# Kernel tuning notes

Hardware: AMD Instinct MI355X
Metric: run time of the kernel (lower is better)

The kernel has to match this reference:

```python
import jax, jax.numpy as jnp
import numpy as np
import math

EMBED_DIM = 1024
NUM_HEADS = 16
HEAD_DIM = EMBED_DIM // NUM_HEADS  # 64
MAX_SEQ_LEN = 2048


def rope_tables(max_seq_len, dim):
    pos = jnp.arange(max_seq_len, dtype=jnp.float32)
    div_term = jnp.exp(jnp.arange(0, dim, 2, dtype=jnp.float32) * -(math.log(10000.0) / dim))
    ang = pos[:, None] * div_term[None, :]  # [S, dim//2]
    return jnp.sin(ang), jnp.cos(ang)


def apply_rope(x, sin, cos):
    # x: [B, H, S, D]; sin/cos: [max_seq, D//2]
    S = x.shape[2]
    sin = sin[:S][None, None]  # [1,1,S,D//2]
    cos = cos[:S][None, None]
    x1, x2 = jnp.split(x, 2, axis=-1)
    return jnp.concatenate([cos * x1 - sin * x2, sin * x1 + cos * x2], axis=-1)


def setup_inputs() -> dict:
    key = jax.random.key(0)
    ks = jax.random.split(key, 5)
    B, S, E = 4, 2048, EMBED_DIM
    std = 1.0 / math.sqrt(E)
    x = jax.random.normal(ks[0], (B, S, E), dtype=jnp.float32)
    Wq = jax.random.normal(ks[1], (E, E), dtype=jnp.float32) * std
    Wk = jax.random.normal(ks[2], (E, E), dtype=jnp.float32) * std
    Wv = jax.random.normal(ks[3], (E, E), dtype=jnp.float32) * std
    Wo = jax.random.normal(ks[4], (E, E), dtype=jnp.float32) * std
    return {"x": x, "Wq": Wq, "Wk": Wk, "Wv": Wv, "Wo": Wo}


def reference(x, Wq, Wk, Wv, Wo):
    B, S, E = x.shape
    H, D = NUM_HEADS, HEAD_DIM
    scale = 1.0 / math.sqrt(D)
    sin, cos = rope_tables(MAX_SEQ_LEN, D)

    def split_heads(t):
        return t.reshape(B, S, H, D).transpose(0, 2, 1, 3)  # [B,H,S,D]

    q = split_heads(x @ Wq)
    k = split_heads(x @ Wk)
    v = split_heads(x @ Wv)
    q = apply_rope(q, sin, cos)
    k = apply_rope(k, sin, cos)

    scores = jnp.einsum('bhqd,bhkd->bhqk', q, k) * scale
    causal = jnp.where(jnp.tril(jnp.ones((S, S), dtype=bool)), 0.0, -1e9)
    scores = scores + causal[None, None]
    attn = jax.nn.softmax(scores, axis=-1)
    out = jnp.einsum('bhqk,bhkd->bhqd', attn, v)  # [B,H,S,D]
    out = out.transpose(0, 2, 1, 3).reshape(B, S, E)
    return out @ Wo
```

## Files before the change

### kernel.cpp

```cpp
#include <hip/hip_runtime.h>

#define DEVFN __device__ __forceinline__

typedef __attribute__((ext_vector_type(8))) short bf16x8;
typedef __attribute__((ext_vector_type(4))) float f32x4;
typedef __attribute__((ext_vector_type(16))) float f32x16;

#define MFMA16(a, b, c) __builtin_amdgcn_mfma_f32_16x16x32_bf16(a, b, c, 0, 0, 0)
#define MFMA32(a, b, c) __builtin_amdgcn_mfma_f32_32x32x16_bf16(a, b, c, 0, 0, 0)

DEVFN unsigned short f2bf(float f) {
  union { float f; unsigned u; } v; v.f = f;
  unsigned r = v.u + 0x7FFFu + ((v.u >> 16) & 1u);
  return (unsigned short)(r >> 16);
}
DEVFN unsigned pack2bf(float a, float b) {
  return (unsigned)f2bf(a) | ((unsigned)f2bf(b) << 16);
}
DEVFN unsigned cvtpk(float lo, float hi) {
  unsigned r;
  asm("v_cvt_pk_bf16_f32 %0, %1, %2" : "=v"(r) : "v"(lo), "v"(hi));
  return r;
}
DEVFN void pl32swap(unsigned& a, unsigned& b) {
  asm("v_permlane32_swap_b32 %0, %1" : "+v"(a), "+v"(b));
}
DEVFN void gll16(const void* g, void* l) {
  __builtin_amdgcn_global_load_lds((__attribute__((address_space(1))) void*)g,
                                   (__attribute__((address_space(3))) void*)l,
                                   16, 0, 0);
}


__global__ __launch_bounds__(256) void conv_x_k(const float* __restrict__ x,
                                                unsigned short* __restrict__ xb) {
  int i = (blockIdx.x * 256 + threadIdx.x) * 4;
  float4 v = *(const float4*)(x + i);
  uint2 u;
  u.x = pack2bf(v.x, v.y);
  u.y = pack2bf(v.z, v.w);
  *(uint2*)(xb + i) = u;
}

__global__ __launch_bounds__(256) void transp_k(
    const float* __restrict__ Wq, const float* __restrict__ Wk,
    const float* __restrict__ Wv, const float* __restrict__ Wo,
    unsigned short* __restrict__ Tq, unsigned short* __restrict__ Tk,
    unsigned short* __restrict__ Tv, unsigned short* __restrict__ To) {
  __shared__ unsigned short t[64 * 65];
  int z = blockIdx.z;
  const float* src = (z == 0) ? Wq : (z == 1) ? Wk : (z == 2) ? Wv : Wo;
  unsigned short* dst = (z == 0) ? Tq : (z == 1) ? Tk : (z == 2) ? Tv : To;
  int k0 = blockIdx.x * 64, n0 = blockIdx.y * 64;
  int tid = threadIdx.x;
#pragma unroll
  for (int i = 0; i < 16; ++i) {
    int flat = i * 256 + tid;
    int r = flat >> 6, cc = flat & 63;
    t[cc * 65 + r] = f2bf(src[(size_t)(k0 + r) * 1024 + n0 + cc]);
  }
  __syncthreads();
#pragma unroll
  for (int i = 0; i < 16; ++i) {
    int flat = i * 256 + tid;
    int rr = flat >> 6, cc = flat & 63;
    dst[(size_t)(n0 + rr) * 1024 + k0 + cc] = t[rr * 65 + cc];
  }
}

__global__ __launch_bounds__(256) void rope_k(float2* __restrict__ rtab) {
  int idx = blockIdx.x * 256 + threadIdx.x;
  int s = idx >> 5, j = idx & 31;
  float freq = expf(-0.28782313714981824f * (float)j);
  float ang = (float)s * freq;
  rtab[idx] = make_float2(sinf(ang), cosf(ang));
}

template <int MODE>
__global__ __launch_bounds__(256) void gemm_k(
    const unsigned short* __restrict__ A, const unsigned short* __restrict__ WT,
    void* __restrict__ outp, const float2* __restrict__ rtab) {
  __shared__ unsigned short At[128 * 64];
  __shared__ unsigned short Bt[128 * 64];
  const int tid = threadIdx.x;
  const int w = tid >> 6, lane = tid & 63, g = lane >> 4, c = lane & 15;
  const int wr = w >> 1, wc = w & 1;
  const int m0 = blockIdx.x * 128, n0 = blockIdx.y * 128;

  f32x4 zero = {0.f, 0.f, 0.f, 0.f};
  f32x4 acc[4][4];
#pragma unroll
  for (int i = 0; i < 4; ++i)
#pragma unroll
    for (int j = 0; j < 4; ++j) acc[i][j] = zero;

  for (int k0 = 0; k0 < 1024; k0 += 64) {
#pragma unroll
    for (int p = 0; p < 4; ++p) {
      int i = p * 256 + tid;
      int row = i >> 3, ls = i & 7;
      size_t off = ((size_t)(m0 + row) * 1024 + k0) * 2 + ((ls ^ (row & 7)) << 4);
      gll16((const char*)A + off, (char*)At + p * 4096 + w * 1024);
      size_t offb = ((size_t)(n0 + row) * 1024 + k0) * 2 + ((ls ^ (row & 7)) << 4);
      gll16((const char*)WT + offb, (char*)Bt + p * 4096 + w * 1024);
    }
    __syncthreads();
#pragma unroll
    for (int ks = 0; ks < 2; ++ks) {
      bf16x8 af[4], bfv[4];
#pragma unroll
      for (int am = 0; am < 4; ++am) {
        int row = wr * 64 + am * 16 + c;
        af[am] = *(const bf16x8*)(At + row * 64 + ((((ks << 2) | g) ^ (row & 7)) << 3));
      }
#pragma unroll
      for (int bn = 0; bn < 4; ++bn) {
        int row = wc * 64 + bn * 16 + c;
        bfv[bn] = *(const bf16x8*)(Bt + row * 64 + ((((ks << 2) | g) ^ (row & 7)) << 3));
      }
#pragma unroll
      for (int am = 0; am < 4; ++am)
#pragma unroll
        for (int bn = 0; bn < 4; ++bn)
          acc[am][bn] = MFMA16(af[am], bfv[bn], acc[am][bn]);
    }
    __syncthreads();
  }

  if (MODE == 0) {
    unsigned short* outb = (unsigned short*)outp;
#pragma unroll
    for (int am = 0; am < 4; ++am)
#pragma unroll
      for (int bp = 0; bp < 2; ++bp) {
        int col = n0 + wc * 64 + bp * 16 + c;
        int h = col >> 6, j = col & 63;
#pragma unroll
        for (int r = 0; r < 4; ++r) {
          int row = m0 + wr * 64 + am * 16 + (g << 2) + r;
          int b = row >> 11, s = row & 2047;
          float x1 = acc[am][bp][r], x2 = acc[am][bp + 2][r];
          float2 sc = rtab[s * 32 + j];
          float o1 = (sc.y * x1 - sc.x * x2) * 0.18033688011112042f;
          float o2 = (sc.x * x1 + sc.y * x2) * 0.18033688011112042f;
          size_t base = (((size_t)(b * 16 + h)) * 2048 + s) * 64;
          outb[base + j] = f2bf(o1);
          outb[base + 32 + j] = f2bf(o2);
        }
      }
  } else if (MODE == 1) {
    unsigned short* outb = (unsigned short*)outp;
#pragma unroll
    for (int am = 0; am < 4; ++am)
#pragma unroll
      for (int bp = 0; bp < 2; ++bp) {
        int col = n0 + wc * 64 + bp * 16 + c;
        int h = col >> 6, j = col & 63;
        const int kb = j >> 4, hil = (j >> 3) & 1, el = j & 7;
#pragma unroll
        for (int r = 0; r < 4; ++r) {
          int row = m0 + wr * 64 + am * 16 + (g << 2) + r;
          int b = row >> 11, s = row & 2047;
          float x1 = acc[am][bp][r], x2 = acc[am][bp + 2][r];
          float2 sc = rtab[s * 32 + j];
          float o1 = sc.y * x1 - sc.x * x2;
          float o2 = sc.x * x1 + sc.y * x2;
          size_t base = (size_t)(b * 16 + h) * 131072 + (size_t)(s >> 5) * 2048 +
                        (hil * 32 + (s & 31)) * 8 + el;
          outb[base + kb * 512] = f2bf(o1);
          outb[base + (kb + 2) * 512] = f2bf(o2);
        }
      }
  } else if (MODE == 2) {
    unsigned short* outb = (unsigned short*)outp;
#pragma unroll
    for (int am = 0; am < 4; ++am)
#pragma unroll
      for (int bn = 0; bn < 4; ++bn) {
        int col = n0 + wc * 64 + bn * 16 + c;
        int h = col >> 6, d = col & 63;
        int row0 = m0 + wr * 64 + am * 16 + (g << 2);
        int b = row0 >> 11, s0 = row0 & 2047;
        uint2 u;
        u.x = pack2bf(acc[am][bn][0], acc[am][bn][1]);
        u.y = pack2bf(acc[am][bn][2], acc[am][bn][3]);
        size_t off = (size_t)(b * 16 + h) * 131072 + (size_t)(s0 >> 6) * 4096 +
                     ((s0 >> 4) & 3) * 1024 + (d >> 5) * 512 +
                     (((s0 >> 3) & 1) * 32 + (d & 31)) * 8 + (s0 & 7);
        *(uint2*)(outb + off) = u;
      }
  } else {
    float* outf = (float*)outp;
#pragma unroll
    for (int am = 0; am < 4; ++am)
#pragma unroll
      for (int bn = 0; bn < 4; ++bn)
#pragma unroll
        for (int r = 0; r < 4; ++r)
          outf[(size_t)(m0 + wr * 64 + am * 16 + (g << 2) + r) * 1024 +
               (n0 + wc * 64 + bn * 16 + c)] = acc[am][bn][r];
  }
}

__global__ __launch_bounds__(256, 2) void attn_k(
    const unsigned short* __restrict__ Q, const unsigned short* __restrict__ Kf,
    const unsigned short* __restrict__ Vf, unsigned short* __restrict__ ctx) {
  const int blk = blockIdx.x;
  const int xcd = blk & 7, idx = blk >> 3;
  const int bh = (xcd << 3) + (idx & 7);
  const int pbase = (idx >> 3) << 2;
  const int tid = threadIdx.x;
  const int w = tid >> 6, lane = tid & 63;
  const int hi = lane >> 5, c5 = lane & 31;
  const int P = pbase + w;

  const unsigned short* Qbh = Q + (size_t)bh * 2048 * 64;
  const unsigned short* Kbh = Kf + (size_t)bh * 131072;
  const unsigned short* Vbh = Vf + (size_t)bh * 131072;
  const int b = bh >> 4, h = bh & 15;

  f32x16 zacc;
#pragma unroll
  for (int i = 0; i < 16; ++i) zacc[i] = 0.f;

  auto pass = [&](int U) {
    const int qw = U * 32;
    const int S = (U >> 1) + 1;

    bf16x8 qf[4];
#pragma unroll
    for (int kb = 0; kb < 4; ++kb)
      qf[kb] = *(const bf16x8*)(Qbh + (size_t)(qw + c5) * 64 + kb * 16 + hi * 8);

    f32x16 oacc[2];
    oacc[0] = zacc; oacc[1] = zacc;
    float m_run = -1e30f, l_run = 0.f;

    bf16x8 kfA[2][4], vfA[2][4], kfB[2][4], vfB[2][4];

    auto loadK = [&](int st, bf16x8 (&dst)[2][4]) {
      const unsigned short* kb_ = Kbh + (size_t)st * 4096 + lane * 8;
#pragma unroll
      for (int t = 0; t < 2; ++t)
#pragma unroll
        for (int kb = 0; kb < 4; ++kb)
          dst[t][kb] = *(const bf16x8*)(kb_ + t * 2048 + kb * 512);
    };
    auto loadV = [&](int st, bf16x8 (&dst)[2][4]) {
      const unsigned short* vb_ = Vbh + (size_t)st * 4096 + lane * 8;
#pragma unroll
      for (int kb = 0; kb < 4; ++kb) {
        dst[0][kb] = *(const bf16x8*)(vb_ + kb * 1024);
        dst[1][kb] = *(const bf16x8*)(vb_ + kb * 1024 + 512);
      }
    };

    auto step = [&](int st, bf16x8 (&kfC)[2][4], bf16x8 (&vfC)[2][4],
                    bf16x8 (&kfN)[2][4], bf16x8 (&vfN)[2][4]) {
      f32x16 sacc[2];
      __builtin_amdgcn_s_setprio(1);
#pragma unroll
      for (int t = 0; t < 2; ++t) {
        sacc[t] = MFMA32(kfC[t][0], qf[0], zacc);
#pragma unroll
        for (int kb = 1; kb < 4; ++kb)
          sacc[t] = MFMA32(kfC[t][kb], qf[kb], sacc[t]);
      }
      __builtin_amdgcn_s_setprio(0);

      if (st + 1 < S) {
        loadK(st + 1, kfN);
        loadV(st + 1, vfN);
      }

      if (st == S - 1) {
        const int q = qw + c5;
#pragma unroll
        for (int t = 0; t < 2; ++t) {
          const int kvb = st * 64 + t * 32 + (hi << 2);
#pragma unroll
          for (int i = 0; i < 16; ++i) {
            int kv = kvb + (i & 3) + ((i >> 2) << 3);
            if (kv > q) sacc[t][i] = -1e30f;
          }
        }
      }

      float vmax = fmaxf(sacc[0][0], sacc[0][1]);
#pragma unroll
      for (int t = 0; t < 2; ++t)
#pragma unroll
        for (int i = (t == 0 ? 2 : 0); i < 16; i += 2)
          vmax = fmaxf(vmax, fmaxf(sacc[t][i], sacc[t][i + 1]));
      vmax = fmaxf(vmax, __shfl_xor(vmax, 32, 64));
      if (!__all(vmax <= m_run + 8.0f)) {
        float m_new = fmaxf(m_run, vmax);
        float alpha = exp2f(m_run - m_new);
        l_run *= alpha;
#pragma unroll
        for (int i = 0; i < 16; ++i) {
          oacc[0][i] *= alpha;
          oacc[1][i] *= alpha;
        }
        m_run = m_new;
      }
      float psum = 0.f;
#pragma unroll
      for (int t = 0; t < 2; ++t)
#pragma unroll
        for (int i = 0; i < 16; ++i) {
          float pv = exp2f(sacc[t][i] - m_run);
          sacc[t][i] = pv;
          psum += pv;
        }
      psum += __shfl_xor(psum, 32, 64);
      l_run += psum;

      unsigned pword[4][4];
#pragma unroll
      for (int t = 0; t < 2; ++t) {
        unsigned X[4][2];
#pragma unroll
        for (int u2 = 0; u2 < 4; ++u2)
#pragma unroll
          for (int wp = 0; wp < 2; ++wp)
            X[u2][wp] = cvtpk(sacc[t][u2 * 4 + 2 * wp], sacc[t][u2 * 4 + 2 * wp + 1]);
#pragma unroll
        for (int par = 0; par < 2; ++par) {
          const int kb = 2 * t + par;
#pragma unroll
          for (int wp = 0; wp < 2; ++wp) {
            unsigned a = X[2 * par][wp], b2 = X[2 * par + 1][wp];
            pl32swap(a, b2);
            pword[kb][wp] = a;
            pword[kb][wp + 2] = b2;
          }
        }
      }

      __builtin_amdgcn_s_setprio(1);
#pragma unroll
      for (int kb = 0; kb < 4; ++kb) {
        union { unsigned u[4]; bf16x8 v; } pw;
#pragma unroll
        for (int k2 = 0; k2 < 4; ++k2) pw.u[k2] = pword[kb][k2];
        oacc[0] = MFMA32(vfC[0][kb], pw.v, oacc[0]);
        oacc[1] = MFMA32(vfC[1][kb], pw.v, oacc[1]);
      }
      __builtin_amdgcn_s_setprio(0);
    };

    loadK(0, kfA);
    loadV(0, vfA);
    for (int st = 0; st < S; st += 2) {
      step(st, kfA, vfA, kfB, vfB);
      if (st + 1 < S) step(st + 1, kfB, vfB, kfA, vfA);
    }

    const float linv = 1.f / l_run;
    unsigned short* crow = ctx + ((size_t)(b * 2048 + qw + c5)) * 1024 + h * 64;
#pragma unroll
    for (int dt = 0; dt < 2; ++dt)
#pragma unroll
      for (int u = 0; u < 4; ++u) {
        int d0 = dt * 32 + 8 * u + 4 * hi;
        uint2 o;
        o.x = cvtpk(oacc[dt][4 * u] * linv, oacc[dt][4 * u + 1] * linv);
        o.y = cvtpk(oacc[dt][4 * u + 2] * linv, oacc[dt][4 * u + 3] * linv);
        *(uint2*)(crow + d0) = o;
      }
  };

  pass(P);
  pass(63 - P);
}


extern "C" void kernel_launch(void* const* d_in, const int* in_sizes, int n_in,
                              void* d_out, int out_size, void* d_ws, size_t ws_size,
                              hipStream_t stream) {
  (void)in_sizes; (void)n_in; (void)out_size; (void)ws_size;
  const float* x = (const float*)d_in[0];
  const float* Wq = (const float*)d_in[1];
  const float* Wk = (const float*)d_in[2];
  const float* Wv = (const float*)d_in[3];
  const float* Wo = (const float*)d_in[4];
  char* ws = (char*)d_ws;
  const size_t MiB = 1024 * 1024;
  unsigned short* xb  = (unsigned short*)(ws);
  unsigned short* WTq = (unsigned short*)(ws + 16 * MiB);
  unsigned short* WTk = (unsigned short*)(ws + 18 * MiB);
  unsigned short* WTv = (unsigned short*)(ws + 20 * MiB);
  unsigned short* WTo = (unsigned short*)(ws + 22 * MiB);
  unsigned short* Qb  = (unsigned short*)(ws + 24 * MiB);
  unsigned short* Kfb = (unsigned short*)(ws + 40 * MiB);
  unsigned short* Vfb = (unsigned short*)(ws + 56 * MiB);
  unsigned short* ctx = (unsigned short*)(ws + 72 * MiB);
  float2* rtab = (float2*)(ws + 88 * MiB);

  conv_x_k<<<8192, 256, 0, stream>>>(x, xb);
  transp_k<<<dim3(16, 16, 4), 256, 0, stream>>>(Wq, Wk, Wv, Wo, WTq, WTk, WTv, WTo);
  rope_k<<<256, 256, 0, stream>>>(rtab);
  gemm_k<0><<<dim3(64, 8), 256, 0, stream>>>(xb, WTq, Qb, rtab);
  gemm_k<1><<<dim3(64, 8), 256, 0, stream>>>(xb, WTk, Kfb, rtab);
  gemm_k<2><<<dim3(64, 8), 256, 0, stream>>>(xb, WTv, Vfb, rtab);
  attn_k<<<512, 256, 0, stream>>>(Qb, Kfb, Vfb, ctx);
  gemm_k<3><<<dim3(64, 8), 256, 0, stream>>>(ctx, WTo, d_out, rtab);
}
```

Measured before the change: 184.4 us.

## Fuse QKV GEMM launches and rebalance causal attention work across blocks

The three Q/K/V projection GEMMs become a single launch with a 64x24 grid that picks the weight matrix and epilogue from blockIdx.y. Attention moves from 512 blocks, each running two balanced passes per wave, to 1024 blocks where the four waves of a block share one query-tile pair index and span two heads. Blocks are ordered so the longest causal tiles are issued first. This aims to cut launch gaps and the tail between dependent GEMMs and to raise occupancy and scheduling balance in attention. The cost is that waves within a block now carry unequal work (U=2s versus 2s+1), and the light-first pairing of the old scheme is dropped.

```diff
diff --git a/kernel.cpp b/kernel.cpp
--- a/kernel.cpp
+++ b/kernel.cpp
@@ -76,16 +76,19 @@
   rtab[idx] = make_float2(sinf(ang), cosf(ang));
 }
 
-template <int MODE>
-__global__ __launch_bounds__(256) void gemm_k(
-    const unsigned short* __restrict__ A, const unsigned short* __restrict__ WT,
-    void* __restrict__ outp, const float2* __restrict__ rtab) {
+__global__ __launch_bounds__(256) void gemm_qkv_k(
+    const unsigned short* __restrict__ A, const unsigned short* __restrict__ WTq,
+    const unsigned short* __restrict__ WTk, const unsigned short* __restrict__ WTv,
+    unsigned short* __restrict__ Qb, unsigned short* __restrict__ Kfb,
+    unsigned short* __restrict__ Vfb, const float2* __restrict__ rtab) {
   __shared__ unsigned short At[128 * 64];
   __shared__ unsigned short Bt[128 * 64];
   const int tid = threadIdx.x;
   const int w = tid >> 6, lane = tid & 63, g = lane >> 4, c = lane & 15;
   const int wr = w >> 1, wc = w & 1;
-  const int m0 = blockIdx.x * 128, n0 = blockIdx.y * 128;
+  const int which = blockIdx.y >> 3;
+  const unsigned short* WT = (which == 0) ? WTq : (which == 1) ? WTk : WTv;
+  const int m0 = blockIdx.x * 128, n0 = (blockIdx.y & 7) * 128;
 
   f32x4 zero = {0.f, 0.f, 0.f, 0.f};
   f32x4 acc[4][4];
@@ -127,8 +130,7 @@
     __syncthreads();
   }
 
-  if (MODE == 0) {
-    unsigned short* outb = (unsigned short*)outp;
+  if (which == 0) {
 #pragma unroll
     for (int am = 0; am < 4; ++am)
 #pragma unroll
@@ -144,12 +146,11 @@
           float o1 = (sc.y * x1 - sc.x * x2) * 0.18033688011112042f;
           float o2 = (sc.x * x1 + sc.y * x2) * 0.18033688011112042f;
           size_t base = (((size_t)(b * 16 + h)) * 2048 + s) * 64;
-          outb[base + j] = f2bf(o1);
-          outb[base + 32 + j] = f2bf(o2);
+          Qb[base + j] = f2bf(o1);
+          Qb[base + 32 + j] = f2bf(o2);
         }
       }
-  } else if (MODE == 1) {
-    unsigned short* outb = (unsigned short*)outp;
+  } else if (which == 1) {
 #pragma unroll
     for (int am = 0; am < 4; ++am)
 #pragma unroll
@@ -167,12 +168,11 @@
           float o2 = sc.x * x1 + sc.y * x2;
           size_t base = (size_t)(b * 16 + h) * 131072 + (size_t)(s >> 5) * 2048 +
                         (hil * 32 + (s & 31)) * 8 + el;
-          outb[base + kb * 512] = f2bf(o1);
-          outb[base + (kb + 2) * 512] = f2bf(o2);
+          Kfb[base + kb * 512] = f2bf(o1);
+          Kfb[base + (kb + 2) * 512] = f2bf(o2);
         }
       }
-  } else if (MODE == 2) {
-    unsigned short* outb = (unsigned short*)outp;
+  } else {
 #pragma unroll
     for (int am = 0; am < 4; ++am)
 #pragma unroll
@@ -187,32 +187,85 @@
         size_t off = (size_t)(b * 16 + h) * 131072 + (size_t)(s0 >> 6) * 4096 +
                      ((s0 >> 4) & 3) * 1024 + (d >> 5) * 512 +
                      (((s0 >> 3) & 1) * 32 + (d & 31)) * 8 + (s0 & 7);
-        *(uint2*)(outb + off) = u;
-      }
-  } else {
-    float* outf = (float*)outp;
-#pragma unroll
-    for (int am = 0; am < 4; ++am)
-#pragma unroll
-      for (int bn = 0; bn < 4; ++bn)
-#pragma unroll
-        for (int r = 0; r < 4; ++r)
-          outf[(size_t)(m0 + wr * 64 + am * 16 + (g << 2) + r) * 1024 +
-               (n0 + wc * 64 + bn * 16 + c)] = acc[am][bn][r];
-  }
+        *(uint2*)(Vfb + off) = u;
+      }
+  }
+}
+
+__global__ __launch_bounds__(256) void gemm_o_k(
+    const unsigned short* __restrict__ A, const unsigned short* __restrict__ WT,
+    float* __restrict__ outf) {
+  __shared__ unsigned short At[128 * 64];
+  __shared__ unsigned short Bt[128 * 64];
+  const int tid = threadIdx.x;
+  const int w = tid >> 6, lane = tid & 63, g = lane >> 4, c = lane & 15;
+  const int wr = w >> 1, wc = w & 1;
+  const int m0 = blockIdx.x * 128, n0 = blockIdx.y * 128;
+
+  f32x4 zero = {0.f, 0.f, 0.f, 0.f};
+  f32x4 acc[4][4];
+#pragma unroll
+  for (int i = 0; i < 4; ++i)
+#pragma unroll
+    for (int j = 0; j < 4; ++j) acc[i][j] = zero;
+
+  for (int k0 = 0; k0 < 1024; k0 += 64) {
+#pragma unroll
+    for (int p = 0; p < 4; ++p) {
+      int i = p * 256 + tid;
+      int row = i >> 3, ls = i & 7;
+      size_t off = ((size_t)(m0 + row) * 1024 + k0) * 2 + ((ls ^ (row & 7)) << 4);
+      gll16((const char*)A + off, (char*)At + p * 4096 + w * 1024);
+      size_t offb = ((size_t)(n0 + row) * 1024 + k0) * 2 + ((ls ^ (row & 7)) << 4);
+      gll16((const char*)WT + offb, (char*)Bt + p * 4096 + w * 1024);
+    }
+    __syncthreads();
+#pragma unroll
+    for (int ks = 0; ks < 2; ++ks) {
+      bf16x8 af[4], bfv[4];
+#pragma unroll
+      for (int am = 0; am < 4; ++am) {
+        int row = wr * 64 + am * 16 + c;
+        af[am] = *(const bf16x8*)(At + row * 64 + ((((ks << 2) | g) ^ (row & 7)) << 3));
+      }
+#pragma unroll
+      for (int bn = 0; bn < 4; ++bn) {
+        int row = wc * 64 + bn * 16 + c;
+        bfv[bn] = *(const bf16x8*)(Bt + row * 64 + ((((ks << 2) | g) ^ (row & 7)) << 3));
+      }
+#pragma unroll
+      for (int am = 0; am < 4; ++am)
+#pragma unroll
+        for (int bn = 0; bn < 4; ++bn)
+          acc[am][bn] = MFMA16(af[am], bfv[bn], acc[am][bn]);
+    }
+    __syncthreads();
+  }
+
+#pragma unroll
+  for (int am = 0; am < 4; ++am)
+#pragma unroll
+    for (int bn = 0; bn < 4; ++bn)
+#pragma unroll
+      for (int r = 0; r < 4; ++r)
+        outf[(size_t)(m0 + wr * 64 + am * 16 + (g << 2) + r) * 1024 +
+             (n0 + wc * 64 + bn * 16 + c)] = acc[am][bn][r];
 }
 
 __global__ __launch_bounds__(256, 2) void attn_k(
     const unsigned short* __restrict__ Q, const unsigned short* __restrict__ Kf,
     const unsigned short* __restrict__ Vf, unsigned short* __restrict__ ctx) {
   const int blk = blockIdx.x;
-  const int xcd = blk & 7, idx = blk >> 3;
-  const int bh = (xcd << 3) + (idx & 7);
-  const int pbase = (idx >> 3) << 2;
+  const int xcd = blk & 7, j = blk >> 3;
+  const int hp = j & 3;
+  const int s = 31 - (j >> 2);
   const int tid = threadIdx.x;
   const int w = tid >> 6, lane = tid & 63;
   const int hi = lane >> 5, c5 = lane & 31;
-  const int P = pbase + w;
+  const int bh = xcd * 8 + hp * 2 + (w & 1);
+  const int U = 2 * s + (w >> 1);
+  const int S = s + 1;
+  const int qw = U * 32;
 
   const unsigned short* Qbh = Q + (size_t)bh * 2048 * 64;
   const unsigned short* Kbh = Kf + (size_t)bh * 131072;
@@ -223,156 +276,148 @@
 #pragma unroll
   for (int i = 0; i < 16; ++i) zacc[i] = 0.f;
 
-  auto pass = [&](int U) {
-    const int qw = U * 32;
-    const int S = (U >> 1) + 1;
-
-    bf16x8 qf[4];
-#pragma unroll
-    for (int kb = 0; kb < 4; ++kb)
-      qf[kb] = *(const bf16x8*)(Qbh + (size_t)(qw + c5) * 64 + kb * 16 + hi * 8);
-
-    f32x16 oacc[2];
-    oacc[0] = zacc; oacc[1] = zacc;
-    float m_run = -1e30f, l_run = 0.f;
-
-    bf16x8 kfA[2][4], vfA[2][4], kfB[2][4], vfB[2][4];
-
-    auto loadK = [&](int st, bf16x8 (&dst)[2][4]) {
-      const unsigned short* kb_ = Kbh + (size_t)st * 4096 + lane * 8;
-#pragma unroll
-      for (int t = 0; t < 2; ++t)
-#pragma unroll
-        for (int kb = 0; kb < 4; ++kb)
-          dst[t][kb] = *(const bf16x8*)(kb_ + t * 2048 + kb * 512);
-    };
-    auto loadV = [&](int st, bf16x8 (&dst)[2][4]) {
-      const unsigned short* vb_ = Vbh + (size_t)st * 4096 + lane * 8;
-#pragma unroll
-      for (int kb = 0; kb < 4; ++kb) {
-        dst[0][kb] = *(const bf16x8*)(vb_ + kb * 1024);
-        dst[1][kb] = *(const bf16x8*)(vb_ + kb * 1024 + 512);
-      }
-    };
-
-    auto step = [&](int st, bf16x8 (&kfC)[2][4], bf16x8 (&vfC)[2][4],
-                    bf16x8 (&kfN)[2][4], bf16x8 (&vfN)[2][4]) {
-      f32x16 sacc[2];
-      __builtin_amdgcn_s_setprio(1);
+  bf16x8 qf[4];
+#pragma unroll
+  for (int kb = 0; kb < 4; ++kb)
+    qf[kb] = *(const bf16x8*)(Qbh + (size_t)(qw + c5) * 64 + kb * 16 + hi * 8);
+
+  f32x16 oacc[2];
+  oacc[0] = zacc; oacc[1] = zacc;
+  float m_run = -1e30f, l_run = 0.f;
+
+  bf16x8 kfA[2][4], vfA[2][4], kfB[2][4], vfB[2][4];
+
+  auto loadK = [&](int st, bf16x8 (&dst)[2][4]) {
+    const unsigned short* kb_ = Kbh + (size_t)st * 4096 + lane * 8;
+#pragma unroll
+    for (int t = 0; t < 2; ++t)
+#pragma unroll
+      for (int kb = 0; kb < 4; ++kb)
+        dst[t][kb] = *(const bf16x8*)(kb_ + t * 2048 + kb * 512);
+  };
+  auto loadV = [&](int st, bf16x8 (&dst)[2][4]) {
+    const unsigned short* vb_ = Vbh + (size_t)st * 4096 + lane * 8;
+#pragma unroll
+    for (int kb = 0; kb < 4; ++kb) {
+      dst[0][kb] = *(const bf16x8*)(vb_ + kb * 1024);
+      dst[1][kb] = *(const bf16x8*)(vb_ + kb * 1024 + 512);
+    }
+  };
+
+  auto step = [&](int st, bf16x8 (&kfC)[2][4], bf16x8 (&vfC)[2][4],
+                  bf16x8 (&kfN)[2][4], bf16x8 (&vfN)[2][4]) {
+    f32x16 sacc[2];
+    __builtin_amdgcn_s_setprio(1);
+#pragma unroll
+    for (int t = 0; t < 2; ++t) {
+      sacc[t] = MFMA32(kfC[t][0], qf[0], zacc);
+#pragma unroll
+      for (int kb = 1; kb < 4; ++kb)
+        sacc[t] = MFMA32(kfC[t][kb], qf[kb], sacc[t]);
+    }
+    __builtin_amdgcn_s_setprio(0);
+
+    if (st + 1 < S) {
+      loadK(st + 1, kfN);
+      loadV(st + 1, vfN);
+    }
+
+    if (st == S - 1) {
+      const int q = qw + c5;
 #pragma unroll
       for (int t = 0; t < 2; ++t) {
-        sacc[t] = MFMA32(kfC[t][0], qf[0], zacc);
-#pragma unroll
-        for (int kb = 1; kb < 4; ++kb)
-          sacc[t] = MFMA32(kfC[t][kb], qf[kb], sacc[t]);
-      }
-      __builtin_amdgcn_s_setprio(0);
-
-      if (st + 1 < S) {
-        loadK(st + 1, kfN);
-        loadV(st + 1, vfN);
-      }
-
-      if (st == S - 1) {
-        const int q = qw + c5;
-#pragma unroll
-        for (int t = 0; t < 2; ++t) {
-          const int kvb = st * 64 + t * 32 + (hi << 2);
-#pragma unroll
-          for (int i = 0; i < 16; ++i) {
-            int kv = kvb + (i & 3) + ((i >> 2) << 3);
-            if (kv > q) sacc[t][i] = -1e30f;
-          }
+        const int kvb = st * 64 + t * 32 + (hi << 2);
+#pragma unroll
+        for (int i = 0; i < 16; ++i) {
+          int kv = kvb + (i & 3) + ((i >> 2) << 3);
+          if (kv > q) sacc[t][i] = -1e30f;
         }
       }
-
-      float vmax = fmaxf(sacc[0][0], sacc[0][1]);
-#pragma unroll
-      for (int t = 0; t < 2; ++t)
-#pragma unroll
-        for (int i = (t == 0 ? 2 : 0); i < 16; i += 2)
-          vmax = fmaxf(vmax, fmaxf(sacc[t][i], sacc[t][i + 1]));
-      vmax = fmaxf(vmax, __shfl_xor(vmax, 32, 64));
-      if (!__all(vmax <= m_run + 8.0f)) {
-        float m_new = fmaxf(m_run, vmax);
-        float alpha = exp2f(m_run - m_new);
-        l_run *= alpha;
-#pragma unroll
-        for (int i = 0; i < 16; ++i) {
-          oacc[0][i] *= alpha;
-          oacc[1][i] *= alpha;
+    }
+
+    float vmax = fmaxf(sacc[0][0], sacc[0][1]);
+#pragma unroll
+    for (int t = 0; t < 2; ++t)
+#pragma unroll
+      for (int i = (t == 0 ? 2 : 0); i < 16; i += 2)
+        vmax = fmaxf(vmax, fmaxf(sacc[t][i], sacc[t][i + 1]));
+    vmax = fmaxf(vmax, __shfl_xor(vmax, 32, 64));
+    if (!__all(vmax <= m_run + 8.0f)) {
+      float m_new = fmaxf(m_run, vmax);
+      float alpha = exp2f(m_run - m_new);
+      l_run *= alpha;
+#pragma unroll
+      for (int i = 0; i < 16; ++i) {
+        oacc[0][i] *= alpha;
+        oacc[1][i] *= alpha;
+      }
+      m_run = m_new;
+    }
+    float psum = 0.f;
+#pragma unroll
+    for (int t = 0; t < 2; ++t)
+#pragma unroll
+      for (int i = 0; i < 16; ++i) {
+        float pv = exp2f(sacc[t][i] - m_run);
+        sacc[t][i] = pv;
+        psum += pv;
+      }
+    psum += __shfl_xor(psum, 32, 64);
+    l_run += psum;
+
+    unsigned pword[4][4];
+#pragma unroll
+    for (int t = 0; t < 2; ++t) {
+      unsigned X[4][2];
+#pragma unroll
+      for (int u2 = 0; u2 < 4; ++u2)
+#pragma unroll
+        for (int wp = 0; wp < 2; ++wp)
+          X[u2][wp] = cvtpk(sacc[t][u2 * 4 + 2 * wp], sacc[t][u2 * 4 + 2 * wp + 1]);
+#pragma unroll
+      for (int par = 0; par < 2; ++par) {
+        const int kb = 2 * t + par;
+#pragma unroll
+        for (int wp = 0; wp < 2; ++wp) {
+          unsigned a = X[2 * par][wp], b2 = X[2 * par + 1][wp];
+          pl32swap(a, b2);
+          pword[kb][wp] = a;
+          pword[kb][wp + 2] = b2;
         }
-        m_run = m_new;
-      }
-      float psum = 0.f;
-#pragma unroll
-      for (int t = 0; t < 2; ++t)
-#pragma unroll
-        for (int i = 0; i < 16; ++i) {
-          float pv = exp2f(sacc[t][i] - m_run);
-          sacc[t][i] = pv;
-          psum += pv;
-        }
-      psum += __shfl_xor(psum, 32, 64);
-      l_run += psum;
-
-      unsigned pword[4][4];
-#pragma unroll
-      for (int t = 0; t < 2; ++t) {
-        unsigned X[4][2];
-#pragma unroll
-        for (int u2 = 0; u2 < 4; ++u2)
-#pragma unroll
-          for (int wp = 0; wp < 2; ++wp)
-            X[u2][wp] = cvtpk(sacc[t][u2 * 4 + 2 * wp], sacc[t][u2 * 4 + 2 * wp + 1]);
-#pragma unroll
-        for (int par = 0; par < 2; ++par) {
-          const int kb = 2 * t + par;
-#pragma unroll
-          for (int wp = 0; wp < 2; ++wp) {
-            unsigned a = X[2 * par][wp], b2 = X[2 * par + 1][wp];
-            pl32swap(a, b2);
-            pword[kb][wp] = a;
-            pword[kb][wp + 2] = b2;
-          }
-        }
-      }
-
-      __builtin_amdgcn_s_setprio(1);
-#pragma unroll
-      for (int kb = 0; kb < 4; ++kb) {
-        union { unsigned u[4]; bf16x8 v; } pw;
-#pragma unroll
-        for (int k2 = 0; k2 < 4; ++k2) pw.u[k2] = pword[kb][k2];
-        oacc[0] = MFMA32(vfC[0][kb], pw.v, oacc[0]);
-        oacc[1] = MFMA32(vfC[1][kb], pw.v, oacc[1]);
-      }
-      __builtin_amdgcn_s_setprio(0);
-    };
-
-    loadK(0, kfA);
-    loadV(0, vfA);
-    for (int st = 0; st < S; st += 2) {
-      step(st, kfA, vfA, kfB, vfB);
-      if (st + 1 < S) step(st + 1, kfB, vfB, kfA, vfA);
-    }
-
-    const float linv = 1.f / l_run;
-    unsigned short* crow = ctx + ((size_t)(b * 2048 + qw + c5)) * 1024 + h * 64;
-#pragma unroll
-    for (int dt = 0; dt < 2; ++dt)
-#pragma unroll
-      for (int u = 0; u < 4; ++u) {
-        int d0 = dt * 32 + 8 * u + 4 * hi;
-        uint2 o;
-        o.x = cvtpk(oacc[dt][4 * u] * linv, oacc[dt][4 * u + 1] * linv);
-        o.y = cvtpk(oacc[dt][4 * u + 2] * linv, oacc[dt][4 * u + 3] * linv);
-        *(uint2*)(crow + d0) = o;
-      }
+      }
+    }
+
+    __builtin_amdgcn_s_setprio(1);
+#pragma unroll
+    for (int kb = 0; kb < 4; ++kb) {
+      union { unsigned u[4]; bf16x8 v; } pw;
+#pragma unroll
+      for (int k2 = 0; k2 < 4; ++k2) pw.u[k2] = pword[kb][k2];
+      oacc[0] = MFMA32(vfC[0][kb], pw.v, oacc[0]);
+      oacc[1] = MFMA32(vfC[1][kb], pw.v, oacc[1]);
+    }
+    __builtin_amdgcn_s_setprio(0);
   };
 
-  pass(P);
-  pass(63 - P);
+  loadK(0, kfA);
+  loadV(0, vfA);
+  for (int st = 0; st < S; st += 2) {
+    step(st, kfA, vfA, kfB, vfB);
+    if (st + 1 < S) step(st + 1, kfB, vfB, kfA, vfA);
+  }
+
+  const float linv = 1.f / l_run;
+  unsigned short* crow = ctx + ((size_t)(b * 2048 + qw + c5)) * 1024 + h * 64;
+#pragma unroll
+  for (int dt = 0; dt < 2; ++dt)
+#pragma unroll
+    for (int u = 0; u < 4; ++u) {
+      int d0 = dt * 32 + 8 * u + 4 * hi;
+      uint2 o;
+      o.x = cvtpk(oacc[dt][4 * u] * linv, oacc[dt][4 * u + 1] * linv);
+      o.y = cvtpk(oacc[dt][4 * u + 2] * linv, oacc[dt][4 * u + 3] * linv);
+      *(uint2*)(crow + d0) = o;
+    }
 }
 
 
@@ -401,9 +446,7 @@
   conv_x_k<<<8192, 256, 0, stream>>>(x, xb);
   transp_k<<<dim3(16, 16, 4), 256, 0, stream>>>(Wq, Wk, Wv, Wo, WTq, WTk, WTv, WTo);
   rope_k<<<256, 256, 0, stream>>>(rtab);
-  gemm_k<0><<<dim3(64, 8), 256, 0, stream>>>(xb, WTq, Qb, rtab);
-  gemm_k<1><<<dim3(64, 8), 256, 0, stream>>>(xb, WTk, Kfb, rtab);
-  gemm_k<2><<<dim3(64, 8), 256, 0, stream>>>(xb, WTv, Vfb, rtab);
-  attn_k<<<512, 256, 0, stream>>>(Qb, Kfb, Vfb, ctx);
-  gemm_k<3><<<dim3(64, 8), 256, 0, stream>>>(ctx, WTo, d_out, rtab);
-}
+  gemm_qkv_k<<<dim3(64, 24), 256, 0, stream>>>(xb, WTq, WTk, WTv, Qb, Kfb, Vfb, rtab);
+  attn_k<<<1024, 256, 0, stream>>>(Qb, Kfb, Vfb, ctx);
+  gemm_o_k<<<dim3(64, 8), 256, 0, stream>>>(ctx, WTo, (float*)d_out);
+}
```

Measured after the change: 178.1 us. 1.04x faster.
